# Optimization experiments

Hardware: AMD Instinct MI355X
Metric: run time of the kernel (lower is better)

Reference implementation:

```python
import jax, jax.numpy as jnp
import numpy as np

B, V, H, W, D = 1, 3, 256, 320, 128
FH, FW, FC = H // 4, W // 4, 32


def conv2d(x, w, b=None, stride=1):
    # 3x3 conv, torch-style padding=1
    y = jax.lax.conv_general_dilated(x, w, (stride, stride), ((1, 1), (1, 1)),
                                     dimension_numbers=('NCHW', 'OIHW', 'NCHW'))
    return y if b is None else y + b[None, :, None, None]


def group_norm(x, gamma, beta, groups, eps=1e-5):
    n, c, h, w = x.shape
    xg = x.reshape(n, groups, c // groups, h, w)
    mu = xg.mean(axis=(2, 3, 4), keepdims=True)
    var = xg.var(axis=(2, 3, 4), keepdims=True)
    xg = (xg - mu) * jax.lax.rsqrt(var + eps)
    return xg.reshape(n, c, h, w) * gamma[None, :, None, None] + beta[None, :, None, None]


def setup_inputs():
    key = jax.random.key(0)
    ks = iter(jax.random.split(key, 64))

    def nrm(shape, scale):
        return jax.random.normal(next(ks), shape, jnp.float32) * scale

    inp = {}
    inp['img_list'] = nrm((B, V, 3, H, W), 1.0)
    # plausible cameras: identity rotations, views translated along x; intrinsics at feature res
    cam = np.zeros((B, V, 2, 4, 4), np.float32)
    K = np.array([[160., 0., 40.], [0., 160., 32.], [0., 0., 1.]], np.float32)
    for v in range(V):
        cam[:, v, 0] = np.eye(4, dtype=np.float32)
        cam[:, v, 0, 0, 3] = 10.0 * v
        cam[:, v, 1, :3, :3] = K
    cam[:, 0, 1, 3, :] = [425.0, 2.5, float(D), 425.0 + 2.5 * (D - 1)]
    inp['cam_params_list'] = jnp.asarray(cam)
    # UNetDS2GN-style extractor: 3 conv-GN-relu stages (stride 1,2,2) + final conv, out 32ch @ 1/4
    inp['fe_w0'] = nrm((8, 3, 3, 3), 0.2); inp['fe_g0'] = jnp.ones(8); inp['fe_b0'] = jnp.zeros(8)
    inp['fe_w1'] = nrm((16, 8, 3, 3), 0.12); inp['fe_g1'] = jnp.ones(16); inp['fe_b1'] = jnp.zeros(16)
    inp['fe_w2'] = nrm((32, 16, 3, 3), 0.08); inp['fe_g2'] = jnp.ones(32); inp['fe_b2'] = jnp.zeros(32)
    inp['fe_w3'] = nrm((32, 32, 3, 3), 0.06); inp['fe_b3'] = jnp.zeros(32)
    # stacked ConvGRUs 32->16->4->2, 3x3 kernels
    for i, (ci, co) in enumerate([(FC, 16), (16, 4), (4, 2)]):
        s = 1.0 / np.sqrt(9.0 * (ci + co))
        for g in ('z', 'r', 'c'):
            inp['gru%d_w%s' % (i, g)] = nrm((co, ci + co, 3, 3), s)
            inp['gru%d_b%s' % (i, g)] = jnp.zeros(co)
    inp['prob_w'] = nrm((1, 2, 3, 3), 0.2)
    inp['prob_b'] = jnp.zeros(1)
    return inp


def reference(img_list, cam_params_list,
              fe_w0, fe_g0, fe_b0, fe_w1, fe_g1, fe_b1, fe_w2, fe_g2, fe_b2, fe_w3, fe_b3,
              gru0_wz, gru0_bz, gru0_wr, gru0_br, gru0_wc, gru0_bc,
              gru1_wz, gru1_bz, gru1_wr, gru1_br, gru1_wc, gru1_bc,
              gru2_wz, gru2_bz, gru2_wr, gru2_br, gru2_wc, gru2_bc,
              prob_w, prob_b):
    cam = cam_params_list
    Rm = cam[:, :, 0, :3, :3]                      # (B,V,3,3)
    t = cam[:, :, 0, :3, 3:4]                      # (B,V,3,1)
    Km = cam[:, :, 1, :3, :3]                      # (B,V,3,3)
    ds = cam[:, 0, 1, 3, 0]; di = cam[:, 0, 1, 3, 1]; de = cam[:, 0, 1, 3, 3]
    depths = jnp.linspace(ds, de, D, axis=-1)      # (B,D)

    # ---- feature extraction over all B*V images ----
    x = img_list.reshape(B * V, 3, H, W)
    x = jax.nn.relu(group_norm(conv2d(x, fe_w0), fe_g0, fe_b0, 1))
    x = jax.nn.relu(group_norm(conv2d(x, fe_w1, stride=2), fe_g1, fe_b1, 2))
    x = jax.nn.relu(group_norm(conv2d(x, fe_w2, stride=2), fe_g2, fe_b2, 4))
    feats = conv2d(x, fe_w3, fe_b3).reshape(B, V, FC, FH, FW)

    # ---- reference-camera rays -> world points (depth-major then pixel, as torch .view) ----
    yy, xx = jnp.meshgrid(jnp.arange(FH, dtype=jnp.float32) + 0.5,
                          jnp.arange(FW, dtype=jnp.float32) + 0.5, indexing='ij')
    grid = jnp.stack([xx.ravel(), yy.ravel(), jnp.ones(FH * FW, jnp.float32)], 0)  # (3,HW)
    uv = jnp.einsum('bij,jn->bin', jnp.linalg.inv(Km[:, 0]), grid)                 # (B,3,HW)
    cam_pts = (uv[:, :, None, :] * depths[:, None, :, None]).reshape(B, 3, -1)     # (B,3,D*HW)
    world = jnp.einsum('bij,bjn->bin', jnp.linalg.inv(Rm[:, 0]), cam_pts - t[:, 0])

    # ---- project into every view + bilinear feature fetch (FeatureFetcher) ----
    p = jnp.einsum('bvij,bjn->bvin', Rm, world) + t
    uvw = jnp.einsum('bvij,bvjn->bvin', Km, p)
    z = uvw[:, :, 2]
    ix = uvw[:, :, 0] / (z + 1e-9) - 0.5
    iy = uvw[:, :, 1] / (z + 1e-9) - 0.5

    def sample(feat, x_, y_):
        # feat: (C,FH,FW); x_,y_: (N,) array coords; zero padding outside
        x0 = jnp.floor(x_); y0 = jnp.floor(y_)
        out = jnp.zeros((FC, x_.shape[0]), x_.dtype)
        for dy in (0.0, 1.0):
            for dx in (0.0, 1.0):
                xc = x0 + dx; yc = y0 + dy
                wgt = (1.0 - jnp.abs(x_ - xc)) * (1.0 - jnp.abs(y_ - yc))
                inb = (xc >= 0) & (xc <= FW - 1) & (yc >= 0) & (yc <= FH - 1)
                xi = jnp.clip(xc, 0, FW - 1).astype(jnp.int32)
                yi = jnp.clip(yc, 0, FH - 1).astype(jnp.int32)
                out = out + feat[:, yi, xi] * (wgt * inb)[None]
        return out

    pf = jax.vmap(sample)(feats.reshape(B * V, FC, FH, FW),
                          ix.reshape(B * V, -1), iy.reshape(B * V, -1))
    pf = pf.reshape(B, V, FC, -1)
    ref_feat = jnp.broadcast_to(feats[:, 0, :, None], (B, FC, D, FH, FW)).reshape(B, FC, -1)
    pf = pf.at[:, 0].set(ref_feat)

    # variance cost volume across views
    cost_volume = ((pf ** 2).mean(1) - pf.mean(1) ** 2).reshape(B, FC, D, FH, FW)

    def gru(x_, h, wz, bz, wr, br, wc, bc):
        xh = jnp.concatenate([x_, h], axis=1)
        zg = jax.nn.sigmoid(conv2d(xh, wz, bz))
        rg = jax.nn.sigmoid(conv2d(xh, wr, br))
        cg = jnp.tanh(conv2d(jnp.concatenate([x_, rg * h], axis=1), wc, bc))
        return zg * h + (1.0 - zg) * cg

    def step(carry, cost_d):
        h1, h2, h3 = carry
        h1 = gru(-cost_d, h1, gru0_wz, gru0_bz, gru0_wr, gru0_br, gru0_wc, gru0_bc)
        h2 = gru(h1, h2, gru1_wz, gru1_bz, gru1_wr, gru1_br, gru1_wc, gru1_bc)
        h3 = gru(h2, h3, gru2_wz, gru2_bz, gru2_wr, gru2_br, gru2_wc, gru2_bc)
        reg = conv2d(h3, prob_w, prob_b)           # (B,1,FH,FW)
        return (h1, h2, h3), reg[:, 0]

    init = (jnp.zeros((B, 16, FH, FW)), jnp.zeros((B, 4, FH, FW)), jnp.zeros((B, 2, FH, FW)))
    _, seq = jax.lax.scan(step, init, jnp.moveaxis(cost_volume, 2, 0))   # (D,B,FH,FW)
    prob_volume = jax.nn.softmax(jnp.moveaxis(seq, 0, 1), axis=1)        # (B,D,FH,FW)

    pred_depth = jnp.einsum('bd,bdhw->bhw', depths, prob_volume)[:, None]  # (B,1,FH,FW)

    idx = (pred_depth[:, 0] - ds[:, None, None]) / di[:, None, None]
    i0 = jnp.floor(idx).astype(jnp.int32)
    gi = jnp.clip(i0[:, None] + jnp.array([-1, 0, 1, 2])[None, :, None, None], 0, D - 1)
    prob_map = jnp.take_along_axis(prob_volume, gi, axis=1).sum(axis=1, keepdims=True)
    return pred_depth, prob_map
```

## Files before the change

kernel.cpp:

```cpp
#include <hip/hip_runtime.h>
#include <hip/hip_bf16.h>
#include <math.h>

#define IMGS 3
#define H0 256
#define W0 320
#define H1 128
#define W1 160
#define FHh 64
#define FWw 80
#define NPIX 5120
#define ND 128
#define FC 32

__device__ inline float ldx(const float* p) { return *p; }
__device__ inline float ldx(const __hip_bfloat16* p) { return __bfloat162float(*p); }
__device__ inline void stx(float* p, float v) { *p = v; }
__device__ inline void stx(__hip_bfloat16* p, float v) { *p = __float2bfloat16(v); }

__device__ inline void inv3(const float* a, float* o) {
    float det = a[0]*(a[4]*a[8]-a[5]*a[7]) - a[1]*(a[3]*a[8]-a[5]*a[6]) + a[2]*(a[3]*a[7]-a[4]*a[6]);
    float id = 1.f/det;
    o[0]=(a[4]*a[8]-a[5]*a[7])*id; o[1]=(a[2]*a[7]-a[1]*a[8])*id; o[2]=(a[1]*a[5]-a[2]*a[4])*id;
    o[3]=(a[5]*a[6]-a[3]*a[8])*id; o[4]=(a[0]*a[8]-a[2]*a[6])*id; o[5]=(a[2]*a[3]-a[0]*a[5])*id;
    o[6]=(a[3]*a[7]-a[4]*a[6])*id; o[7]=(a[1]*a[6]-a[0]*a[7])*id; o[8]=(a[0]*a[4]-a[1]*a[3])*id;
}
__device__ inline void mm3(const float* A, const float* B, float* C) {
    for (int i=0;i<3;i++) for (int j=0;j<3;j++)
        C[i*3+j] = A[i*3+0]*B[0*3+j] + A[i*3+1]*B[1*3+j] + A[i*3+2]*B[2*3+j];
}
__device__ inline void mv3(const float* A, const float* x, float* y) {
    for (int i=0;i<3;i++) y[i] = A[i*3+0]*x[0]+A[i*3+1]*x[1]+A[i*3+2]*x[2];
}

__global__ void k_setup(const float* __restrict__ cam, float* __restrict__ su) {
    if (threadIdx.x != 0 || blockIdx.x != 0) return;
    auto at = [&](int v,int e,int i,int j){ return cam[(v*2+e)*16 + i*4 + j]; };
    float R0[9], K0[9], t0[3], iR0[9], iK0[9];
    for (int i=0;i<3;i++){
        for (int j=0;j<3;j++){ R0[i*3+j]=at(0,0,i,j); K0[i*3+j]=at(0,1,i,j); }
        t0[i]=at(0,0,i,3);
    }
    inv3(R0,iR0); inv3(K0,iK0);
    float ds = at(0,1,3,0), di = at(0,1,3,1), de = at(0,1,3,3);
    for (int d=0; d<ND; d++) su[48+d] = ds + (de-ds)*(float)d/(float)(ND-1);
    su[176]=ds; su[177]=di;
    for (int v=0; v<3; v++){
        float Rv[9], Kv[9], tv[3];
        for (int i=0;i<3;i++){
            for (int j=0;j<3;j++){ Rv[i*3+j]=at(v,0,i,j); Kv[i*3+j]=at(v,1,i,j); }
            tv[i]=at(v,0,i,3);
        }
        float A[9], KA[9], M[9];
        mm3(Rv, iR0, A); mm3(Kv, A, KA); mm3(KA, iK0, M);
        float At0[3], tmp[3], bv[3];
        mv3(A, t0, At0);
        for (int i=0;i<3;i++) tmp[i]=tv[i]-At0[i];
        mv3(Kv, tmp, bv);
        for (int i=0;i<9;i++) su[v*12+i]=M[i];
        for (int i=0;i<3;i++) su[v*12+9+i]=bv[i];
    }
}

__global__ __launch_bounds__(256) void k_conv3x3(
    const float* __restrict__ in, const float* __restrict__ w, const float* __restrict__ bias,
    float* __restrict__ out, int Cin, int Hin, int Win, int Cout, int Hout, int Wout, int stride)
{
    int img = blockIdx.y / Cout, co = blockIdx.y % Cout;
    extern __shared__ float wsm[];
    for (int i = threadIdx.x; i < Cin*9; i += 256) wsm[i] = w[co*Cin*9 + i];
    __syncthreads();
    int p = blockIdx.x*256 + threadIdx.x;
    if (p >= Hout*Wout) return;
    int oy = p / Wout, ox = p - oy*Wout;
    const float* ib = in + (size_t)img*Cin*Hin*Win;
    float acc = bias ? bias[co] : 0.f;
    for (int ky=0; ky<3; ky++){
        int iy = oy*stride - 1 + ky;
        if ((unsigned)iy >= (unsigned)Hin) continue;
        for (int kx=0; kx<3; kx++){
            int ix = ox*stride - 1 + kx;
            if ((unsigned)ix >= (unsigned)Win) continue;
            const float* ip = ib + (size_t)iy*Win + ix;
            const float* wp = wsm + ky*3 + kx;
            for (int ci=0; ci<Cin; ci++)
                acc = fmaf(wp[ci*9], ip[(size_t)ci*Hin*Win], acc);
        }
    }
    out[((size_t)img*Cout + co)*Hout*Wout + p] = acc;
}

__global__ __launch_bounds__(256) void k_gnstats(
    const float* __restrict__ x, float* __restrict__ stats, int Cg, int HW)
{
    const float* p = x + (size_t)blockIdx.x * Cg * HW;
    int M = Cg*HW;
    float s1=0.f, s2=0.f;
    for (int i=threadIdx.x; i<M; i+=256){ float v=p[i]; s1+=v; s2=fmaf(v,v,s2); }
    __shared__ float a1[256], a2[256];
    a1[threadIdx.x]=s1; a2[threadIdx.x]=s2; __syncthreads();
    for (int s=128; s>0; s>>=1){
        if (threadIdx.x < s){ a1[threadIdx.x]+=a1[threadIdx.x+s]; a2[threadIdx.x]+=a2[threadIdx.x+s]; }
        __syncthreads();
    }
    if (threadIdx.x==0){
        float mean = a1[0]/(float)M;
        float var  = a2[0]/(float)M - mean*mean;
        stats[blockIdx.x*2]   = mean;
        stats[blockIdx.x*2+1] = rsqrtf(var + 1e-5f);
    }
}

__global__ __launch_bounds__(256) void k_gnapply(
    float* __restrict__ x, const float* __restrict__ stats,
    const float* __restrict__ gamma, const float* __restrict__ beta,
    int C, int HW, int CgHW, int total)
{
    int i = blockIdx.x*256 + threadIdx.x;
    if (i >= total) return;
    int ch  = (i / HW) % C;
    int grp = i / CgHW;
    float mean = stats[grp*2], rstd = stats[grp*2+1];
    float v = (x[i]-mean)*rstd*gamma[ch] + beta[ch];
    x[i] = fmaxf(v, 0.f);
}

__global__ __launch_bounds__(256) void k_transpose(
    const float* __restrict__ f, float* __restrict__ ft)
{
    int i = blockIdx.x*256 + threadIdx.x;
    if (i >= IMGS*FC*NPIX) return;
    int n = i % NPIX;
    int c = (i / NPIX) % FC;
    int im = i / (FC*NPIX);
    ft[((size_t)im*NPIX + n)*FC + c] = f[i];
}

template<typename TO>
__global__ __launch_bounds__(256) void k_warpcost(
    const float* __restrict__ ft, const float* __restrict__ su, TO* __restrict__ xb)
{
    int t = blockIdx.x*256 + threadIdx.x;
    int d = t / NPIX, n = t - d*NPIX;
    int py = n / FWw, px = n - py*FWw;
    float u = px + 0.5f, v = py + 0.5f;
    float depth = su[48 + d];
    float s1[FC], s2[FC], samp[FC];
    const float* f0 = ft + (size_t)n*FC;
#pragma unroll
    for (int c=0;c<FC;c++){ float f = f0[c]; s1[c] = f; s2[c] = f*f; }
    for (int vv=1; vv<3; vv++){
        const float* m = su + vv*12;
        float wx = fmaf(fmaf(m[0],u,fmaf(m[1],v,m[2])), depth, m[9]);
        float wy = fmaf(fmaf(m[3],u,fmaf(m[4],v,m[5])), depth, m[10]);
        float wz = fmaf(fmaf(m[6],u,fmaf(m[7],v,m[8])), depth, m[11]);
        float iz = 1.f/(wz + 1e-9f);
        float ix = wx*iz - 0.5f, iy = wy*iz - 0.5f;
        float x0 = floorf(ix), y0 = floorf(iy);
#pragma unroll
        for (int c=0;c<FC;c++) samp[c] = 0.f;
        const float* fv = ft + (size_t)vv*NPIX*FC;
        for (int dy=0; dy<2; dy++){
            for (int dx=0; dx<2; dx++){
                float xc = x0+(float)dx, yc = y0+(float)dy;
                if (xc < 0.f || xc > (float)(FWw-1) || yc < 0.f || yc > (float)(FHh-1)) continue;
                float wgt = (1.f - fabsf(ix-xc))*(1.f - fabsf(iy-yc));
                const float* fp = fv + ((size_t)((int)yc)*FWw + (int)xc)*FC;
#pragma unroll
                for (int c=0;c<FC;c++) samp[c] = fmaf(fp[c], wgt, samp[c]);
            }
        }
#pragma unroll
        for (int c=0;c<FC;c++){ s1[c] += samp[c]; s2[c] = fmaf(samp[c], samp[c], s2[c]); }
    }
    TO* ob = xb + (size_t)d*FC*NPIX + n;
#pragma unroll
    for (int c=0;c<FC;c++){
        float m1 = s1[c]*(1.f/3.f);
        float cost = s2[c]*(1.f/3.f) - m1*m1;
        stx(ob + (size_t)c*NPIX, -cost);
    }
}

template<typename TX, int CX, int CH>
__global__ __launch_bounds__(256) void k_gru_zr(
    const TX* __restrict__ x, const float* __restrict__ h,
    const float* __restrict__ wz, const float* __restrict__ bz,
    const float* __restrict__ wr, const float* __restrict__ br,
    float* __restrict__ zg, float* __restrict__ rh)
{
    int n = blockIdx.x*256 + threadIdx.x;
    int co = blockIdx.y;
    int py = n / FWw, px = n - py*FWw;
    const float* wzc = wz + (size_t)co*(CX+CH)*9;
    const float* wrc = wr + (size_t)co*(CX+CH)*9;
    float az = bz[co], ar = br[co];
#pragma unroll
    for (int ky=0; ky<3; ky++){
        int iy = py + ky - 1;
        if ((unsigned)iy >= (unsigned)FHh) continue;
#pragma unroll
        for (int kx=0; kx<3; kx++){
            int ixp = px + kx - 1;
            if ((unsigned)ixp >= (unsigned)FWw) continue;
            int off = iy*FWw + ixp;
            int k = ky*3 + kx;
#pragma unroll
            for (int ci=0; ci<CX; ci++){
                float vx = ldx(x + (size_t)ci*NPIX + off);
                az = fmaf(wzc[ci*9+k], vx, az);
                ar = fmaf(wrc[ci*9+k], vx, ar);
            }
#pragma unroll
            for (int ci=0; ci<CH; ci++){
                float vh = h[(size_t)ci*NPIX + off];
                az = fmaf(wzc[(CX+ci)*9+k], vh, az);
                ar = fmaf(wrc[(CX+ci)*9+k], vh, ar);
            }
        }
    }
    float z = 1.f/(1.f + expf(-az));
    float r = 1.f/(1.f + expf(-ar));
    zg[(size_t)co*NPIX + n] = z;
    rh[(size_t)co*NPIX + n] = r * h[(size_t)co*NPIX + n];
}

template<typename TX, int CX, int CH>
__global__ __launch_bounds__(256) void k_gru_c(
    const TX* __restrict__ x, const float* __restrict__ rh, const float* __restrict__ hold,
    const float* __restrict__ wc, const float* __restrict__ bc,
    const float* __restrict__ zg, float* __restrict__ hnew)
{
    int n = blockIdx.x*256 + threadIdx.x;
    int co = blockIdx.y;
    int py = n / FWw, px = n - py*FWw;
    const float* wcc = wc + (size_t)co*(CX+CH)*9;
    float ac = bc[co];
#pragma unroll
    for (int ky=0; ky<3; ky++){
        int iy = py + ky - 1;
        if ((unsigned)iy >= (unsigned)FHh) continue;
#pragma unroll
        for (int kx=0; kx<3; kx++){
            int ixp = px + kx - 1;
            if ((unsigned)ixp >= (unsigned)FWw) continue;
            int off = iy*FWw + ixp;
            int k = ky*3 + kx;
#pragma unroll
            for (int ci=0; ci<CX; ci++){
                float vx = ldx(x + (size_t)ci*NPIX + off);
                ac = fmaf(wcc[ci*9+k], vx, ac);
            }
#pragma unroll
            for (int ci=0; ci<CH; ci++){
                float vh = rh[(size_t)ci*NPIX + off];
                ac = fmaf(wcc[(CX+ci)*9+k], vh, ac);
            }
        }
    }
    float cg = tanhf(ac);
    float z = zg[(size_t)co*NPIX + n];
    hnew[(size_t)co*NPIX + n] = z*hold[(size_t)co*NPIX + n] + (1.f - z)*cg;
}

__global__ __launch_bounds__(256) void k_prob(
    const float* __restrict__ h3, const float* __restrict__ w, const float* __restrict__ b,
    float* __restrict__ reg)
{
    int n = blockIdx.x*256 + threadIdx.x;
    int py = n / FWw, px = n - py*FWw;
    float a = b[0];
#pragma unroll
    for (int ky=0; ky<3; ky++){
        int iy = py + ky - 1;
        if ((unsigned)iy >= (unsigned)FHh) continue;
#pragma unroll
        for (int kx=0; kx<3; kx++){
            int ixp = px + kx - 1;
            if ((unsigned)ixp >= (unsigned)FWw) continue;
            int off = iy*FWw + ixp;
            int k = ky*3 + kx;
            a = fmaf(w[k],   h3[off],        a);
            a = fmaf(w[9+k], h3[NPIX+off],   a);
        }
    }
    reg[n] = a;
}

__global__ __launch_bounds__(256) void k_final(
    const float* __restrict__ reg, const float* __restrict__ su, float* __restrict__ out)
{
    int n = blockIdx.x*256 + threadIdx.x;
    if (n >= NPIX) return;
    float m = -1e30f;
    for (int d=0; d<ND; d++) m = fmaxf(m, reg[(size_t)d*NPIX + n]);
    float s = 0.f, acc = 0.f;
    for (int d=0; d<ND; d++){
        float e = expf(reg[(size_t)d*NPIX + n] - m);
        s += e;
        acc = fmaf(e, su[48+d], acc);
    }
    float inv_s = 1.f/s;
    float pred = acc * inv_s;
    float ds = su[176], di = su[177];
    int i0 = (int)floorf((pred - ds)/di);
    float pm = 0.f;
    for (int k=0; k<4; k++){
        int g = min(max(i0 - 1 + k, 0), ND-1);
        pm += expf(reg[(size_t)g*NPIX + n] - m);
    }
    pm *= inv_s;
    out[n]        = pred;
    out[NPIX + n] = pm;
}

extern "C" void kernel_launch(void* const* d_in, const int* in_sizes, int n_in,
                              void* d_out, int out_size, void* d_ws, size_t ws_size,
                              hipStream_t stream)
{
    (void)in_sizes; (void)n_in; (void)out_size;
    const float* img   = (const float*)d_in[0];
    const float* cam   = (const float*)d_in[1];
    const float* fe_w0 = (const float*)d_in[2];
    const float* fe_g0 = (const float*)d_in[3];
    const float* fe_b0 = (const float*)d_in[4];
    const float* fe_w1 = (const float*)d_in[5];
    const float* fe_g1 = (const float*)d_in[6];
    const float* fe_b1 = (const float*)d_in[7];
    const float* fe_w2 = (const float*)d_in[8];
    const float* fe_g2 = (const float*)d_in[9];
    const float* fe_b2 = (const float*)d_in[10];
    const float* fe_w3 = (const float*)d_in[11];
    const float* fe_b3 = (const float*)d_in[12];
    const float* gw[3][3]; const float* gb[3][3];
    for (int i=0;i<3;i++) for (int g=0; g<3; g++){
        gw[i][g] = (const float*)d_in[13 + i*6 + g*2];
        gb[i][g] = (const float*)d_in[13 + i*6 + g*2 + 1];
    }
    const float* prob_w = (const float*)d_in[31];
    const float* prob_b = (const float*)d_in[32];
    float* out = (float*)d_out;

    char* base = (char*)d_ws;
    size_t off = 0;
    auto alloc = [&](size_t bytes)->char*{
        char* p = base + off; off += (bytes + 255) & ~(size_t)255; return p;
    };
    float* su     = (float*)alloc(256*4);
    float* stats  = (float*)alloc(64*4);
    float* buf0   = (float*)alloc((size_t)IMGS*8*H0*W0*4);
    float* buf1   = (float*)alloc((size_t)IMGS*16*H1*W1*4);
    float* buf2   = (float*)alloc((size_t)IMGS*32*NPIX*4);
    float* feats  = (float*)alloc((size_t)IMGS*32*NPIX*4);
    float* featst = (float*)alloc((size_t)IMGS*NPIX*FC*4);
    float* reg    = (float*)alloc((size_t)ND*NPIX*4);
    float* h1[2]; h1[0]=(float*)alloc(16*NPIX*4); h1[1]=(float*)alloc(16*NPIX*4);
    float* h2[2]; h2[0]=(float*)alloc(4*NPIX*4);  h2[1]=(float*)alloc(4*NPIX*4);
    float* h3[2]; h3[0]=(float*)alloc(2*NPIX*4);  h3[1]=(float*)alloc(2*NPIX*4);
    float* zg0 = (float*)alloc(16*NPIX*4);
    float* rh0 = (float*)alloc(16*NPIX*4);
    float* zg1 = (float*)alloc(4*NPIX*4);
    float* rh1 = (float*)alloc(4*NPIX*4);
    float* zg2 = (float*)alloc(2*NPIX*4);
    float* rh2 = (float*)alloc(2*NPIX*4);
    size_t off_common = off;
    bool xf32 = (ws_size >= off_common + (size_t)ND*FC*NPIX*4);
    void* xbuf = (void*)(base + off_common);

    hipMemsetAsync(h1[0], 0, 16*NPIX*4, stream);
    hipMemsetAsync(h2[0], 0, 4*NPIX*4, stream);
    hipMemsetAsync(h3[0], 0, 2*NPIX*4, stream);

    k_setup<<<1, 64, 0, stream>>>(cam, su);

    k_conv3x3<<<dim3((H0*W0+255)/256, IMGS*8), 256, 3*9*4, stream>>>(
        img, fe_w0, nullptr, buf0, 3, H0, W0, 8, H0, W0, 1);
    k_gnstats<<<IMGS*1, 256, 0, stream>>>(buf0, stats, 8, H0*W0);
    k_gnapply<<<(IMGS*8*H0*W0+255)/256, 256, 0, stream>>>(
        buf0, stats, fe_g0, fe_b0, 8, H0*W0, 8*H0*W0, IMGS*8*H0*W0);
    k_conv3x3<<<dim3((H1*W1+255)/256, IMGS*16), 256, 8*9*4, stream>>>(
        buf0, fe_w1, nullptr, buf1, 8, H0, W0, 16, H1, W1, 2);
    k_gnstats<<<IMGS*2, 256, 0, stream>>>(buf1, stats, 8, H1*W1);
    k_gnapply<<<(IMGS*16*H1*W1+255)/256, 256, 0, stream>>>(
        buf1, stats, fe_g1, fe_b1, 16, H1*W1, 8*H1*W1, IMGS*16*H1*W1);
    k_conv3x3<<<dim3((NPIX+255)/256, IMGS*32), 256, 16*9*4, stream>>>(
        buf1, fe_w2, nullptr, buf2, 16, H1, W1, 32, FHh, FWw, 2);
    k_gnstats<<<IMGS*4, 256, 0, stream>>>(buf2, stats, 8, NPIX);
    k_gnapply<<<(IMGS*32*NPIX+255)/256, 256, 0, stream>>>(
        buf2, stats, fe_g2, fe_b2, 32, NPIX, 8*NPIX, IMGS*32*NPIX);
    k_conv3x3<<<dim3((NPIX+255)/256, IMGS*32), 256, 32*9*4, stream>>>(
        buf2, fe_w3, fe_b3, feats, 32, FHh, FWw, 32, FHh, FWw, 1);
    k_transpose<<<(IMGS*FC*NPIX+255)/256, 256, 0, stream>>>(feats, featst);

    if (xf32) {
        k_warpcost<float><<<ND*NPIX/256, 256, 0, stream>>>(featst, su, (float*)xbuf);
    } else {
        k_warpcost<__hip_bfloat16><<<ND*NPIX/256, 256, 0, stream>>>(featst, su, (__hip_bfloat16*)xbuf);
    }

    for (int d=0; d<ND; d++){
        int cur = d & 1, nxt = cur ^ 1;
        if (xf32) {
            const float* xd = (const float*)xbuf + (size_t)d*FC*NPIX;
            k_gru_zr<float,32,16><<<dim3(NPIX/256,16),256,0,stream>>>(
                xd, h1[cur], gw[0][0], gb[0][0], gw[0][1], gb[0][1], zg0, rh0);
            k_gru_c<float,32,16><<<dim3(NPIX/256,16),256,0,stream>>>(
                xd, rh0, h1[cur], gw[0][2], gb[0][2], zg0, h1[nxt]);
        } else {
            const __hip_bfloat16* xd = (const __hip_bfloat16*)xbuf + (size_t)d*FC*NPIX;
            k_gru_zr<__hip_bfloat16,32,16><<<dim3(NPIX/256,16),256,0,stream>>>(
                xd, h1[cur], gw[0][0], gb[0][0], gw[0][1], gb[0][1], zg0, rh0);
            k_gru_c<__hip_bfloat16,32,16><<<dim3(NPIX/256,16),256,0,stream>>>(
                xd, rh0, h1[cur], gw[0][2], gb[0][2], zg0, h1[nxt]);
        }
        k_gru_zr<float,16,4><<<dim3(NPIX/256,4),256,0,stream>>>(
            h1[nxt], h2[cur], gw[1][0], gb[1][0], gw[1][1], gb[1][1], zg1, rh1);
        k_gru_c<float,16,4><<<dim3(NPIX/256,4),256,0,stream>>>(
            h1[nxt], rh1, h2[cur], gw[1][2], gb[1][2], zg1, h2[nxt]);
        k_gru_zr<float,4,2><<<dim3(NPIX/256,2),256,0,stream>>>(
            h2[nxt], h3[cur], gw[2][0], gb[2][0], gw[2][1], gb[2][1], zg2, rh2);
        k_gru_c<float,4,2><<<dim3(NPIX/256,2),256,0,stream>>>(
            h2[nxt], rh2, h3[cur], gw[2][2], gb[2][2], zg2, h3[nxt]);
        k_prob<<<dim3(NPIX/256),256,0,stream>>>(h3[nxt], prob_w, prob_b, reg + (size_t)d*NPIX);
    }

    k_final<<<NPIX/256, 256, 0, stream>>>(reg, su, out);
}
```

Before: 8.035 ms.

## Replace per-depth GRU kernel launches with one persistent wavefront-pipelined scan kernel

Replaces the 896 small per-depth GRU and probability-conv launches with a single persistent kernel of 512 blocks that synchronise through a global atomic barrier. The three GRU layers and the probability conv run as a software pipeline offset by one depth step each, so each step needs only two grid barriers. Activations switch to a pixel-major, channel-interleaved layout, and fast exp-based sigmoid and tanh replace the library calls. The prob role recomputes h3's candidate gate redundantly to avoid a third barrier. The design relies on all 512 blocks being co-resident, otherwise the barrier deadlocks.

After: 31.22 ms. 3.89x slower.

```diff
diff --git a/kernel.cpp b/kernel.cpp
--- a/kernel.cpp
+++ b/kernel.cpp
@@ -12,11 +12,15 @@
 #define NPIX 5120
 #define ND 128
 #define FC 32
+#define NBLK 512
 
 __device__ inline float ldx(const float* p) { return *p; }
 __device__ inline float ldx(const __hip_bfloat16* p) { return __bfloat162float(*p); }
 __device__ inline void stx(float* p, float v) { *p = v; }
 __device__ inline void stx(__hip_bfloat16* p, float v) { *p = __float2bfloat16(v); }
+
+__device__ inline float sigm_(float x){ return 1.f/(1.f+__expf(-x)); }
+__device__ inline float tanh_(float x){ return 1.f - 2.f/(__expf(2.f*x)+1.f); }
 
 __device__ inline void inv3(const float* a, float* o) {
     float det = a[0]*(a[4]*a[8]-a[5]*a[7]) - a[1]*(a[3]*a[8]-a[5]*a[6]) + a[2]*(a[3]*a[7]-a[4]*a[6]);
@@ -173,118 +177,288 @@
 #pragma unroll
         for (int c=0;c<FC;c++){ s1[c] += samp[c]; s2[c] = fmaf(samp[c], samp[c], s2[c]); }
     }
-    TO* ob = xb + (size_t)d*FC*NPIX + n;
+    TO* ob = xb + ((size_t)d*NPIX + n)*FC;
 #pragma unroll
     for (int c=0;c<FC;c++){
         float m1 = s1[c]*(1.f/3.f);
         float cost = s2[c]*(1.f/3.f) - m1*m1;
-        stx(ob + (size_t)c*NPIX, -cost);
-    }
-}
-
-template<typename TX, int CX, int CH>
-__global__ __launch_bounds__(256) void k_gru_zr(
-    const TX* __restrict__ x, const float* __restrict__ h,
-    const float* __restrict__ wz, const float* __restrict__ bz,
-    const float* __restrict__ wr, const float* __restrict__ br,
-    float* __restrict__ zg, float* __restrict__ rh)
-{
-    int n = blockIdx.x*256 + threadIdx.x;
-    int co = blockIdx.y;
-    int py = n / FWw, px = n - py*FWw;
-    const float* wzc = wz + (size_t)co*(CX+CH)*9;
-    const float* wrc = wr + (size_t)co*(CX+CH)*9;
-    float az = bz[co], ar = br[co];
-#pragma unroll
-    for (int ky=0; ky<3; ky++){
-        int iy = py + ky - 1;
-        if ((unsigned)iy >= (unsigned)FHh) continue;
-#pragma unroll
-        for (int kx=0; kx<3; kx++){
-            int ixp = px + kx - 1;
-            if ((unsigned)ixp >= (unsigned)FWw) continue;
-            int off = iy*FWw + ixp;
-            int k = ky*3 + kx;
-#pragma unroll
-            for (int ci=0; ci<CX; ci++){
-                float vx = ldx(x + (size_t)ci*NPIX + off);
-                az = fmaf(wzc[ci*9+k], vx, az);
-                ar = fmaf(wrc[ci*9+k], vx, ar);
-            }
-#pragma unroll
-            for (int ci=0; ci<CH; ci++){
-                float vh = h[(size_t)ci*NPIX + off];
-                az = fmaf(wzc[(CX+ci)*9+k], vh, az);
-                ar = fmaf(wrc[(CX+ci)*9+k], vh, ar);
-            }
+        stx(ob + c, -cost);
+    }
+}
+
+struct ScanArgs {
+    const void* xv;
+    const float *wz1,*bz1,*wr1,*br1,*wc1,*bc1;
+    const float *wz2,*bz2,*wr2,*br2,*wc2,*bc2;
+    const float *wz3,*bz3,*wr3,*br3,*wc3,*bc3;
+    const float *wp,*bp;
+    float *h1a,*h1b,*h2a,*h2b,*h3a,*h3b;
+    float *zg0,*rh0,*zg1,*rh1,*zg2,*rh2;
+    float *reg;
+    unsigned *bar;
+};
+
+__device__ inline void gsync(unsigned* bar)
+{
+    __syncthreads();
+    if (threadIdx.x == 0) {
+        __threadfence();
+        unsigned* cnt = bar;
+        unsigned* gen = bar + 1;
+        unsigned g = __hip_atomic_load(gen, __ATOMIC_RELAXED, __HIP_MEMORY_SCOPE_AGENT);
+        unsigned a = __hip_atomic_fetch_add(cnt, 1u, __ATOMIC_ACQ_REL, __HIP_MEMORY_SCOPE_AGENT);
+        if (a == NBLK - 1u) {
+            __hip_atomic_store(cnt, 0u, __ATOMIC_RELAXED, __HIP_MEMORY_SCOPE_AGENT);
+            __hip_atomic_store(gen, g + 1u, __ATOMIC_RELEASE, __HIP_MEMORY_SCOPE_AGENT);
+        } else {
+            while (__hip_atomic_load(gen, __ATOMIC_RELAXED, __HIP_MEMORY_SCOPE_AGENT) == g)
+                __builtin_amdgcn_s_sleep(2);
         }
-    }
-    float z = 1.f/(1.f + expf(-az));
-    float r = 1.f/(1.f + expf(-ar));
-    zg[(size_t)co*NPIX + n] = z;
-    rh[(size_t)co*NPIX + n] = r * h[(size_t)co*NPIX + n];
-}
-
-template<typename TX, int CX, int CH>
-__global__ __launch_bounds__(256) void k_gru_c(
-    const TX* __restrict__ x, const float* __restrict__ rh, const float* __restrict__ hold,
-    const float* __restrict__ wc, const float* __restrict__ bc,
-    const float* __restrict__ zg, float* __restrict__ hnew)
-{
-    int n = blockIdx.x*256 + threadIdx.x;
-    int co = blockIdx.y;
-    int py = n / FWw, px = n - py*FWw;
-    const float* wcc = wc + (size_t)co*(CX+CH)*9;
-    float ac = bc[co];
-#pragma unroll
-    for (int ky=0; ky<3; ky++){
-        int iy = py + ky - 1;
-        if ((unsigned)iy >= (unsigned)FHh) continue;
-#pragma unroll
-        for (int kx=0; kx<3; kx++){
-            int ixp = px + kx - 1;
-            if ((unsigned)ixp >= (unsigned)FWw) continue;
-            int off = iy*FWw + ixp;
-            int k = ky*3 + kx;
-#pragma unroll
-            for (int ci=0; ci<CX; ci++){
-                float vx = ldx(x + (size_t)ci*NPIX + off);
-                ac = fmaf(wcc[ci*9+k], vx, ac);
-            }
-#pragma unroll
-            for (int ci=0; ci<CH; ci++){
-                float vh = rh[(size_t)ci*NPIX + off];
-                ac = fmaf(wcc[(CX+ci)*9+k], vh, ac);
-            }
+        __threadfence();
+    }
+    __syncthreads();
+}
+
+template<typename TX>
+__global__ __launch_bounds__(256, 2) void k_scan(ScanArgs S)
+{
+    const int bid = blockIdx.x, tid = threadIdx.x;
+    int role, co = 0, n = 0;
+    if      (bid < 320) { role = 0; co = bid/20;        n = (bid%20)*256 + tid; }
+    else if (bid < 400) { role = 1; int i = bid - 320; co = i/20; n = (i%20)*256 + tid; }
+    else if (bid < 440) { role = 2; int i = bid - 400; co = i/20; n = (i%20)*256 + tid; }
+    else if (bid < 460) { role = 3; n = (bid-440)*256 + tid; }
+    else role = 4;
+    const int py = n / FWw, px = n - py*FWw;
+
+    const float *wzc=nullptr, *wrc=nullptr, *wcc=nullptr;
+    float bzv=0.f, brv=0.f, bcv=0.f;
+    if (role == 0){ wzc=S.wz1+co*432; wrc=S.wr1+co*432; wcc=S.wc1+co*432; bzv=S.bz1[co]; brv=S.br1[co]; bcv=S.bc1[co]; }
+    if (role == 1){ wzc=S.wz2+co*180; wrc=S.wr2+co*180; wcc=S.wc2+co*180; bzv=S.bz2[co]; brv=S.br2[co]; bcv=S.bc2[co]; }
+    if (role == 2){ wzc=S.wz3+co*54;  wrc=S.wr3+co*54;  wcc=S.wc3+co*54;  bzv=S.bz3[co]; brv=S.br3[co]; bcv=S.bc3[co]; }
+
+    float zsave = 0.f;
+
+    for (int k = 0; k < ND + 2; ++k) {
+        if (role == 0 && k < ND) {
+            const int d = k;
+            const TX* xd = (const TX*)S.xv + (size_t)d*NPIX*FC;
+            const float* h1o = ((d-1)&1) ? S.h1b : S.h1a;
+            float az = bzv, ar = brv;
+#pragma unroll 1
+            for (int ky=0; ky<3; ky++){
+                int qy = py + ky - 1; if ((unsigned)qy >= (unsigned)FHh) continue;
+#pragma unroll 1
+                for (int kx=0; kx<3; kx++){
+                    int qx = px + kx - 1; if ((unsigned)qx >= (unsigned)FWw) continue;
+                    int q = qy*FWw + qx, j = ky*3 + kx;
+                    const TX* xp = xd + (size_t)q*FC;
+#pragma unroll
+                    for (int ci=0; ci<32; ci++){
+                        float v = ldx(xp + ci);
+                        az = fmaf(wzc[ci*9+j], v, az);
+                        ar = fmaf(wrc[ci*9+j], v, ar);
+                    }
+                    const float* hp = h1o + q*16;
+#pragma unroll
+                    for (int ci=0; ci<16; ci++){
+                        float v = hp[ci];
+                        az = fmaf(wzc[(32+ci)*9+j], v, az);
+                        ar = fmaf(wrc[(32+ci)*9+j], v, ar);
+                    }
+                }
+            }
+            float z = sigm_(az), r = sigm_(ar);
+            zsave = z;
+            S.zg0[n*16+co] = z;
+            S.rh0[n*16+co] = r * h1o[n*16+co];
+        } else if (role == 1 && k >= 1 && k <= ND) {
+            const int d = k - 1;
+            const float* x2  = (d&1) ? S.h1b : S.h1a;
+            const float* h2o = ((d-1)&1) ? S.h2b : S.h2a;
+            float az = bzv, ar = brv;
+#pragma unroll 1
+            for (int ky=0; ky<3; ky++){
+                int qy = py + ky - 1; if ((unsigned)qy >= (unsigned)FHh) continue;
+#pragma unroll 1
+                for (int kx=0; kx<3; kx++){
+                    int qx = px + kx - 1; if ((unsigned)qx >= (unsigned)FWw) continue;
+                    int q = qy*FWw + qx, j = ky*3 + kx;
+                    const float* xp = x2 + q*16;
+#pragma unroll
+                    for (int ci=0; ci<16; ci++){
+                        float v = xp[ci];
+                        az = fmaf(wzc[ci*9+j], v, az);
+                        ar = fmaf(wrc[ci*9+j], v, ar);
+                    }
+                    const float* hp = h2o + q*4;
+#pragma unroll
+                    for (int ci=0; ci<4; ci++){
+                        float v = hp[ci];
+                        az = fmaf(wzc[(16+ci)*9+j], v, az);
+                        ar = fmaf(wrc[(16+ci)*9+j], v, ar);
+                    }
+                }
+            }
+            float z = sigm_(az), r = sigm_(ar);
+            zsave = z;
+            S.zg1[n*4+co] = z;
+            S.rh1[n*4+co] = r * h2o[n*4+co];
+        } else if (role == 2 && k >= 2) {
+            const int d = k - 2;
+            const float* x3  = (d&1) ? S.h2b : S.h2a;
+            const float* h3o = ((d-1)&1) ? S.h3b : S.h3a;
+            float az = bzv, ar = brv;
+#pragma unroll 1
+            for (int ky=0; ky<3; ky++){
+                int qy = py + ky - 1; if ((unsigned)qy >= (unsigned)FHh) continue;
+#pragma unroll 1
+                for (int kx=0; kx<3; kx++){
+                    int qx = px + kx - 1; if ((unsigned)qx >= (unsigned)FWw) continue;
+                    int q = qy*FWw + qx, j = ky*3 + kx;
+                    const float* xp = x3 + q*4;
+#pragma unroll
+                    for (int ci=0; ci<4; ci++){
+                        float v = xp[ci];
+                        az = fmaf(wzc[ci*9+j], v, az);
+                        ar = fmaf(wrc[ci*9+j], v, ar);
+                    }
+                    const float* hp = h3o + q*2;
+#pragma unroll
+                    for (int ci=0; ci<2; ci++){
+                        float v = hp[ci];
+                        az = fmaf(wzc[(4+ci)*9+j], v, az);
+                        ar = fmaf(wrc[(4+ci)*9+j], v, ar);
+                    }
+                }
+            }
+            float z = sigm_(az), r = sigm_(ar);
+            zsave = z;
+            S.zg2[n*2+co] = z;
+            S.rh2[n*2+co] = r * h3o[n*2+co];
         }
-    }
-    float cg = tanhf(ac);
-    float z = zg[(size_t)co*NPIX + n];
-    hnew[(size_t)co*NPIX + n] = z*hold[(size_t)co*NPIX + n] + (1.f - z)*cg;
-}
-
-__global__ __launch_bounds__(256) void k_prob(
-    const float* __restrict__ h3, const float* __restrict__ w, const float* __restrict__ b,
-    float* __restrict__ reg)
-{
-    int n = blockIdx.x*256 + threadIdx.x;
-    int py = n / FWw, px = n - py*FWw;
-    float a = b[0];
-#pragma unroll
-    for (int ky=0; ky<3; ky++){
-        int iy = py + ky - 1;
-        if ((unsigned)iy >= (unsigned)FHh) continue;
-#pragma unroll
-        for (int kx=0; kx<3; kx++){
-            int ixp = px + kx - 1;
-            if ((unsigned)ixp >= (unsigned)FWw) continue;
-            int off = iy*FWw + ixp;
-            int k = ky*3 + kx;
-            a = fmaf(w[k],   h3[off],        a);
-            a = fmaf(w[9+k], h3[NPIX+off],   a);
+        gsync(S.bar);
+
+        if (role == 0 && k < ND) {
+            const int d = k;
+            const TX* xd = (const TX*)S.xv + (size_t)d*NPIX*FC;
+            const float* h1o = ((d-1)&1) ? S.h1b : S.h1a;
+            float*       h1n = (d&1)     ? S.h1b : S.h1a;
+            float ac = bcv;
+#pragma unroll 1
+            for (int ky=0; ky<3; ky++){
+                int qy = py + ky - 1; if ((unsigned)qy >= (unsigned)FHh) continue;
+#pragma unroll 1
+                for (int kx=0; kx<3; kx++){
+                    int qx = px + kx - 1; if ((unsigned)qx >= (unsigned)FWw) continue;
+                    int q = qy*FWw + qx, j = ky*3 + kx;
+                    const TX* xp = xd + (size_t)q*FC;
+#pragma unroll
+                    for (int ci=0; ci<32; ci++)
+                        ac = fmaf(wcc[ci*9+j], ldx(xp + ci), ac);
+                    const float* rp = S.rh0 + q*16;
+#pragma unroll
+                    for (int ci=0; ci<16; ci++)
+                        ac = fmaf(wcc[(32+ci)*9+j], rp[ci], ac);
+                }
+            }
+            float cg = tanh_(ac);
+            float z = zsave;
+            h1n[n*16+co] = z*h1o[n*16+co] + (1.f - z)*cg;
+        } else if (role == 1 && k >= 1 && k <= ND) {
+            const int d = k - 1;
+            const float* x2  = (d&1) ? S.h1b : S.h1a;
+            const float* h2o = ((d-1)&1) ? S.h2b : S.h2a;
+            float*       h2n = (d&1)     ? S.h2b : S.h2a;
+            float ac = bcv;
+#pragma unroll 1
+            for (int ky=0; ky<3; ky++){
+                int qy = py + ky - 1; if ((unsigned)qy >= (unsigned)FHh) continue;
+#pragma unroll 1
+                for (int kx=0; kx<3; kx++){
+                    int qx = px + kx - 1; if ((unsigned)qx >= (unsigned)FWw) continue;
+                    int q = qy*FWw + qx, j = ky*3 + kx;
+                    const float* xp = x2 + q*16;
+#pragma unroll
+                    for (int ci=0; ci<16; ci++)
+                        ac = fmaf(wcc[ci*9+j], xp[ci], ac);
+                    const float* rp = S.rh1 + q*4;
+#pragma unroll
+                    for (int ci=0; ci<4; ci++)
+                        ac = fmaf(wcc[(16+ci)*9+j], rp[ci], ac);
+                }
+            }
+            float cg = tanh_(ac);
+            float z = zsave;
+            h2n[n*4+co] = z*h2o[n*4+co] + (1.f - z)*cg;
+        } else if (role == 2 && k >= 2) {
+            const int d = k - 2;
+            const float* x3  = (d&1) ? S.h2b : S.h2a;
+            const float* h3o = ((d-1)&1) ? S.h3b : S.h3a;
+            float*       h3n = (d&1)     ? S.h3b : S.h3a;
+            float ac = bcv;
+#pragma unroll 1
+            for (int ky=0; ky<3; ky++){
+                int qy = py + ky - 1; if ((unsigned)qy >= (unsigned)FHh) continue;
+#pragma unroll 1
+                for (int kx=0; kx<3; kx++){
+                    int qx = px + kx - 1; if ((unsigned)qx >= (unsigned)FWw) continue;
+                    int q = qy*FWw + qx, j = ky*3 + kx;
+                    const float* xp = x3 + q*4;
+#pragma unroll
+                    for (int ci=0; ci<4; ci++)
+                        ac = fmaf(wcc[ci*9+j], xp[ci], ac);
+                    const float* rp = S.rh2 + q*2;
+                    ac = fmaf(wcc[4*9+j], rp[0], ac);
+                    ac = fmaf(wcc[5*9+j], rp[1], ac);
+                }
+            }
+            float cg = tanh_(ac);
+            float z = zsave;
+            h3n[n*2+co] = z*h3o[n*2+co] + (1.f - z)*cg;
+        } else if (role == 3 && k >= 2) {
+            const int d = k - 2;
+            const float* x3  = (d&1) ? S.h2b : S.h2a;
+            const float* h3o = ((d-1)&1) ? S.h3b : S.h3a;
+            float a = S.bp[0];
+#pragma unroll 1
+            for (int ky=0; ky<3; ky++){
+                int qy = py + ky - 1; if ((unsigned)qy >= (unsigned)FHh) continue;
+#pragma unroll 1
+                for (int kx=0; kx<3; kx++){
+                    int qx = px + kx - 1; if ((unsigned)qx >= (unsigned)FWw) continue;
+                    int q = qy*FWw + qx;
+#pragma unroll 1
+                    for (int c2=0; c2<2; c2++){
+                        const float* wc3c = S.wc3 + c2*54;
+                        float ac = S.bc3[c2];
+#pragma unroll 1
+                        for (int jy=0; jy<3; jy++){
+                            int ry = qy + jy - 1; if ((unsigned)ry >= (unsigned)FHh) continue;
+#pragma unroll 1
+                            for (int jx=0; jx<3; jx++){
+                                int rx = qx + jx - 1; if ((unsigned)rx >= (unsigned)FWw) continue;
+                                int rq = ry*FWw + rx, jj = jy*3 + jx;
+                                const float* xp = x3 + rq*4;
+#pragma unroll
+                                for (int ci=0; ci<4; ci++)
+                                    ac = fmaf(wc3c[ci*9+jj], xp[ci], ac);
+                                const float* rp = S.rh2 + rq*2;
+                                ac = fmaf(wc3c[4*9+jj], rp[0], ac);
+                                ac = fmaf(wc3c[5*9+jj], rp[1], ac);
+                            }
+                        }
+                        float cg = tanh_(ac);
+                        float z = S.zg2[q*2+c2];
+                        float h3n = z*h3o[q*2+c2] + (1.f - z)*cg;
+                        a = fmaf(S.wp[c2*9 + ky*3 + kx], h3n, a);
+                    }
+                }
+            }
+            S.reg[(size_t)d*NPIX + n] = a;
         }
-    }
-    reg[n] = a;
+        gsync(S.bar);
+    }
 }
 
 __global__ __launch_bounds__(256) void k_final(
@@ -348,15 +522,16 @@
     };
     float* su     = (float*)alloc(256*4);
     float* stats  = (float*)alloc(64*4);
+    unsigned* bar = (unsigned*)alloc(2*4);
     float* buf0   = (float*)alloc((size_t)IMGS*8*H0*W0*4);
     float* buf1   = (float*)alloc((size_t)IMGS*16*H1*W1*4);
     float* buf2   = (float*)alloc((size_t)IMGS*32*NPIX*4);
     float* feats  = (float*)alloc((size_t)IMGS*32*NPIX*4);
     float* featst = (float*)alloc((size_t)IMGS*NPIX*FC*4);
     float* reg    = (float*)alloc((size_t)ND*NPIX*4);
-    float* h1[2]; h1[0]=(float*)alloc(16*NPIX*4); h1[1]=(float*)alloc(16*NPIX*4);
-    float* h2[2]; h2[0]=(float*)alloc(4*NPIX*4);  h2[1]=(float*)alloc(4*NPIX*4);
-    float* h3[2]; h3[0]=(float*)alloc(2*NPIX*4);  h3[1]=(float*)alloc(2*NPIX*4);
+    float* h1a = (float*)alloc(16*NPIX*4); float* h1b = (float*)alloc(16*NPIX*4);
+    float* h2a = (float*)alloc(4*NPIX*4);  float* h2b = (float*)alloc(4*NPIX*4);
+    float* h3a = (float*)alloc(2*NPIX*4);  float* h3b = (float*)alloc(2*NPIX*4);
     float* zg0 = (float*)alloc(16*NPIX*4);
     float* rh0 = (float*)alloc(16*NPIX*4);
     float* zg1 = (float*)alloc(4*NPIX*4);
@@ -367,9 +542,10 @@
     bool xf32 = (ws_size >= off_common + (size_t)ND*FC*NPIX*4);
     void* xbuf = (void*)(base + off_common);
 
-    hipMemsetAsync(h1[0], 0, 16*NPIX*4, stream);
-    hipMemsetAsync(h2[0], 0, 4*NPIX*4, stream);
-    hipMemsetAsync(h3[0], 0, 2*NPIX*4, stream);
+    (void)hipMemsetAsync(h1b, 0, 16*NPIX*4, stream);
+    (void)hipMemsetAsync(h2b, 0, 4*NPIX*4, stream);
+    (void)hipMemsetAsync(h3b, 0, 2*NPIX*4, stream);
+    (void)hipMemsetAsync(bar, 0, 2*4, stream);
 
     k_setup<<<1, 64, 0, stream>>>(cam, su);
 
@@ -392,37 +568,20 @@
         buf2, fe_w3, fe_b3, feats, 32, FHh, FWw, 32, FHh, FWw, 1);
     k_transpose<<<(IMGS*FC*NPIX+255)/256, 256, 0, stream>>>(feats, featst);
 
-    if (xf32) {
-        k_warpcost<float><<<ND*NPIX/256, 256, 0, stream>>>(featst, su, (float*)xbuf);
-    } else {
-        k_warpcost<__hip_bfloat16><<<ND*NPIX/256, 256, 0, stream>>>(featst, su, (__hip_bfloat16*)xbuf);
-    }
-
-    for (int d=0; d<ND; d++){
-        int cur = d & 1, nxt = cur ^ 1;
-        if (xf32) {
-            const float* xd = (const float*)xbuf + (size_t)d*FC*NPIX;
-            k_gru_zr<float,32,16><<<dim3(NPIX/256,16),256,0,stream>>>(
-                xd, h1[cur], gw[0][0], gb[0][0], gw[0][1], gb[0][1], zg0, rh0);
-            k_gru_c<float,32,16><<<dim3(NPIX/256,16),256,0,stream>>>(
-                xd, rh0, h1[cur], gw[0][2], gb[0][2], zg0, h1[nxt]);
-        } else {
-            const __hip_bfloat16* xd = (const __hip_bfloat16*)xbuf + (size_t)d*FC*NPIX;
-            k_gru_zr<__hip_bfloat16,32,16><<<dim3(NPIX/256,16),256,0,stream>>>(
-                xd, h1[cur], gw[0][0], gb[0][0], gw[0][1], gb[0][1], zg0, rh0);
-            k_gru_c<__hip_bfloat16,32,16><<<dim3(NPIX/256,16),256,0,stream>>>(
-                xd, rh0, h1[cur], gw[0][2], gb[0][2], zg0, h1[nxt]);
-        }
-        k_gru_zr<float,16,4><<<dim3(NPIX/256,4),256,0,stream>>>(
-            h1[nxt], h2[cur], gw[1][0], gb[1][0], gw[1][1], gb[1][1], zg1, rh1);
-        k_gru_c<float,16,4><<<dim3(NPIX/256,4),256,0,stream>>>(
-            h1[nxt], rh1, h2[cur], gw[1][2], gb[1][2], zg1, h2[nxt]);
-        k_gru_zr<float,4,2><<<dim3(NPIX/256,2),256,0,stream>>>(
-            h2[nxt], h3[cur], gw[2][0], gb[2][0], gw[2][1], gb[2][1], zg2, rh2);
-        k_gru_c<float,4,2><<<dim3(NPIX/256,2),256,0,stream>>>(
-            h2[nxt], rh2, h3[cur], gw[2][2], gb[2][2], zg2, h3[nxt]);
-        k_prob<<<dim3(NPIX/256),256,0,stream>>>(h3[nxt], prob_w, prob_b, reg + (size_t)d*NPIX);
-    }
+    if (xf32) k_warpcost<float><<<ND*NPIX/256, 256, 0, stream>>>(featst, su, (float*)xbuf);
+    else      k_warpcost<__hip_bfloat16><<<ND*NPIX/256, 256, 0, stream>>>(featst, su, (__hip_bfloat16*)xbuf);
+
+    ScanArgs S;
+    S.xv = xbuf;
+    S.wz1=gw[0][0]; S.bz1=gb[0][0]; S.wr1=gw[0][1]; S.br1=gb[0][1]; S.wc1=gw[0][2]; S.bc1=gb[0][2];
+    S.wz2=gw[1][0]; S.bz2=gb[1][0]; S.wr2=gw[1][1]; S.br2=gb[1][1]; S.wc2=gw[1][2]; S.bc2=gb[1][2];
+    S.wz3=gw[2][0]; S.bz3=gb[2][0]; S.wr3=gw[2][1]; S.br3=gb[2][1]; S.wc3=gw[2][2]; S.bc3=gb[2][2];
+    S.wp=prob_w; S.bp=prob_b;
+    S.h1a=h1a; S.h1b=h1b; S.h2a=h2a; S.h2b=h2b; S.h3a=h3a; S.h3b=h3b;
+    S.zg0=zg0; S.rh0=rh0; S.zg1=zg1; S.rh1=rh1; S.zg2=zg2; S.rh2=rh2;
+    S.reg=reg; S.bar=bar;
+    if (xf32) k_scan<float><<<NBLK, 256, 0, stream>>>(S);
+    else      k_scan<__hip_bfloat16><<<NBLK, 256, 0, stream>>>(S);
 
     k_final<<<NPIX/256, 256, 0, stream>>>(reg, su, out);
 }
```
